# Performance work log

Hardware: AMD Instinct MI355X
Metric: run time of the kernel (lower is better)

The kernel has to match this reference:

```python
import jax, jax.numpy as jnp
import numpy as np
from jax import lax


def setup_inputs() -> dict:
    key = jax.random.key(0)
    k1, k2 = jax.random.split(key)
    B, H, W, Cin, Cout, kh, kw = 16, 128, 128, 128, 128, 3, 3
    X = jax.random.normal(k1, (B, H, W, Cin), dtype=jnp.float32)
    kernel = jax.random.normal(k2, (B, kh, kw, Cin, Cout), dtype=jnp.float32) * 0.05
    return {"X": X, "kernel": kernel}


def _conv_one(x, k):
    # x: [H, W, Cin]; k: [kh, kw, Cin, Cout] -> [H', W', Cout]
    out = lax.conv_general_dilated(
        x[None],  # [1, H, W, Cin]
        k,
        window_strides=(1, 1),
        padding='VALID',
        dimension_numbers=('NHWC', 'HWIO', 'NHWC'),
    )
    return out[0]


def reference(X, kernel):
    # Per-sample dynamic-filter conv: each batch element convolved with its own
    # [kh, kw, Cin, Cout] filter. Equivalent to the TF depthwise-reshape trick
    # followed by reduce_sum over the input-channel axis.
    return jax.vmap(_conv_one)(X, kernel)  # [B, H', W', Cout]
```

## Files before the change

kernel.cpp:

```cpp
#include <hip/hip_runtime.h>
#include <cstdint>

#define OWD 126
#define MTOT 15876

typedef short bf16x8 __attribute__((ext_vector_type(8)));
typedef float f32x4  __attribute__((ext_vector_type(4)));

__device__ __forceinline__ uint16_t f2bf(float f) {
    union { float f; uint32_t u; } v;
    v.f = f;
    uint32_t u = v.u;
    return (uint16_t)((u + 0x7FFFu + ((u >> 16) & 1u)) >> 16);
}

__device__ __forceinline__ uint32_t pk2(float a, float b) {
    return (uint32_t)f2bf(a) | ((uint32_t)f2bf(b) << 16);
}

__global__ __launch_bounds__(256) void kprep(const float* __restrict__ Kin,
                                             uint16_t* __restrict__ Bt) {
    const int rs = blockIdx.x;
    const int b  = blockIdx.y;
    const int t  = threadIdx.x;
    const int n  = t & 127;
    const int og = t >> 7;

    const float* src = Kin + (((size_t)b * 9 + rs) << 14);
    uint16_t*    dst = Bt + ((size_t)b * 128 + n) * 1152 + rs * 128;

#pragma unroll
    for (int o = 0; o < 8; ++o) {
        const int oct = og * 8 + o;
        const float* s0 = src + (oct * 8) * 128 + n;
        uint4 p;
        p.x = pk2(s0[0 * 128], s0[1 * 128]);
        p.y = pk2(s0[2 * 128], s0[3 * 128]);
        p.z = pk2(s0[4 * 128], s0[5 * 128]);
        p.w = pk2(s0[6 * 128], s0[7 * 128]);
        *(uint4*)(dst + oct * 8) = p;
    }
}

__global__ __launch_bounds__(256) void conv_mfma(const float* __restrict__ X,
                                                 const uint16_t* __restrict__ Bt,
                                                 float* __restrict__ Out) {
    __shared__ __align__(16) uint16_t lA[128 * 64];
    __shared__ __align__(16) uint16_t lB[128 * 64];

    const int mtile = blockIdx.x;
    const int b     = blockIdx.y;
    const int tid   = threadIdx.x;
    const int lane  = tid & 63;
    const int wave  = tid >> 6;
    const int wm    = (wave & 1) << 6;
    const int wn    = (wave >> 1) << 6;
    const int l15   = lane & 15;
    const int quad  = lane >> 4;

    const int srow  = tid >> 1;
    const int shalf = tid & 1;

    int m = mtile * 128 + srow;
    if (m >= MTOT) m = MTOT - 1;
    const int oh = m / OWD;
    const int ow = m - oh * OWD;
    const float*    Xb = X + (((size_t)b * 128 + oh) * 128 + ow) * 128;
    const uint16_t* Bb = Bt + ((size_t)b * 128 + srow) * 1152 + shalf * 32;

    f32x4 acc[4][4];
#pragma unroll
    for (int i = 0; i < 4; ++i)
#pragma unroll
        for (int j = 0; j < 4; ++j)
            acc[i][j] = (f32x4){0.f, 0.f, 0.f, 0.f};

    for (int chunk = 0; chunk < 18; ++chunk) {
        const int rs = chunk >> 1;
        const int c0 = (chunk & 1) << 6;
        const int r  = rs / 3;
        const int s  = rs - r * 3;

        __syncthreads();

        {
            const float4* src = (const float4*)(Xb + (r * 128 + s) * 128 + c0 + shalf * 32);
            float4 v[8];
#pragma unroll
            for (int i = 0; i < 8; ++i) v[i] = src[i];
#pragma unroll
            for (int i = 0; i < 4; ++i) {
                uint4 p;
                p.x = pk2(v[2 * i].x, v[2 * i].y);
                p.y = pk2(v[2 * i].z, v[2 * i].w);
                p.z = pk2(v[2 * i + 1].x, v[2 * i + 1].y);
                p.w = pk2(v[2 * i + 1].z, v[2 * i + 1].w);
                const int ci = (shalf * 4 + i) ^ (srow & 7);
                *(uint4*)&lA[srow * 64 + ci * 8] = p;
            }
        }
        {
            const uint4* bsrc = (const uint4*)(Bb + rs * 128 + c0);
#pragma unroll
            for (int i = 0; i < 4; ++i) {
                const uint4 p = bsrc[i];
                const int ci = (shalf * 4 + i) ^ (srow & 7);
                *(uint4*)&lB[srow * 64 + ci * 8] = p;
            }
        }

        __syncthreads();

#pragma unroll
        for (int ksub = 0; ksub < 2; ++ksub) {
            bf16x8 af[4], bfr[4];
#pragma unroll
            for (int i = 0; i < 4; ++i) {
                const int row = wm + i * 16 + l15;
                const int ci  = (ksub * 4 + quad) ^ (row & 7);
                af[i] = *(const bf16x8*)&lA[row * 64 + ci * 8];
            }
#pragma unroll
            for (int j = 0; j < 4; ++j) {
                const int row = wn + j * 16 + l15;
                const int ci  = (ksub * 4 + quad) ^ (row & 7);
                bfr[j] = *(const bf16x8*)&lB[row * 64 + ci * 8];
            }
#pragma unroll
            for (int i = 0; i < 4; ++i)
#pragma unroll
                for (int j = 0; j < 4; ++j)
                    acc[i][j] = __builtin_amdgcn_mfma_f32_16x16x32_bf16(
                        af[i], bfr[j], acc[i][j], 0, 0, 0);
        }
    }

#pragma unroll
    for (int i = 0; i < 4; ++i) {
#pragma unroll
        for (int rr = 0; rr < 4; ++rr) {
            const int mrow = mtile * 128 + wm + i * 16 + quad * 4 + rr;
            if (mrow < MTOT) {
                const int oh2 = mrow / OWD;
                const int ow2 = mrow - oh2 * OWD;
                float* op = Out + (((size_t)b * OWD + oh2) * OWD + ow2) * 128 + wn + l15;
#pragma unroll
                for (int j = 0; j < 4; ++j)
                    op[j * 16] = acc[i][j][rr];
            }
        }
    }
}

extern "C" void kernel_launch(void* const* d_in, const int* in_sizes, int n_in,
                              void* d_out, int out_size, void* d_ws, size_t ws_size,
                              hipStream_t stream) {
    const float* X   = (const float*)d_in[0];
    const float* Kin = (const float*)d_in[1];
    float*       Out = (float*)d_out;
    uint16_t*    Bt  = (uint16_t*)d_ws;

    kprep<<<dim3(9, 16), 256, 0, stream>>>(Kin, Bt);
    conv_mfma<<<dim3(125, 16), 256, 0, stream>>>(X, Bt, Out);
}
```

Measured before the change: 387.0 us.

## Pre-convert X to bf16 and stream tiles via global_load_lds

```diff
diff --git a/kernel.cpp b/kernel.cpp
--- a/kernel.cpp
+++ b/kernel.cpp
@@ -6,6 +6,10 @@
 
 typedef short bf16x8 __attribute__((ext_vector_type(8)));
 typedef float f32x4  __attribute__((ext_vector_type(4)));
+
+#define BT_ELEMS  (16u * 128u * 1152u)
+#define XBF_ELEMS (16u * 128u * 128u * 128u)
+#define WS_NEEDED ((size_t)(BT_ELEMS + XBF_ELEMS) * 2)
 
 __device__ __forceinline__ uint16_t f2bf(float f) {
     union { float f; uint32_t u; } v;
@@ -16,6 +20,12 @@
 
 __device__ __forceinline__ uint32_t pk2(float a, float b) {
     return (uint32_t)f2bf(a) | ((uint32_t)f2bf(b) << 16);
+}
+
+__device__ __forceinline__ void gl_lds16(const uint16_t* g, uint16_t* l) {
+    __builtin_amdgcn_global_load_lds(
+        (const __attribute__((address_space(1))) uint32_t*)g,
+        (__attribute__((address_space(3))) uint32_t*)l, 16, 0, 0);
 }
 
 __global__ __launch_bounds__(256) void kprep(const float* __restrict__ Kin,
@@ -42,11 +52,24 @@
     }
 }
 
-__global__ __launch_bounds__(256) void conv_mfma(const float* __restrict__ X,
-                                                 const uint16_t* __restrict__ Bt,
-                                                 float* __restrict__ Out) {
-    __shared__ __align__(16) uint16_t lA[128 * 64];
-    __shared__ __align__(16) uint16_t lB[128 * 64];
+__global__ __launch_bounds__(256) void xprep(const float* __restrict__ X,
+                                             uint16_t* __restrict__ Xbf) {
+    const size_t i = ((size_t)blockIdx.x * 256 + threadIdx.x) * 8;
+    const float4 a = *(const float4*)(X + i);
+    const float4 b = *(const float4*)(X + i + 4);
+    uint4 p;
+    p.x = pk2(a.x, a.y);
+    p.y = pk2(a.z, a.w);
+    p.z = pk2(b.x, b.y);
+    p.w = pk2(b.z, b.w);
+    *(uint4*)(Xbf + i) = p;
+}
+
+__global__ __launch_bounds__(256) void conv_mfma_a(const uint16_t* __restrict__ Xbf,
+                                                   const uint16_t* __restrict__ Bt,
+                                                   float* __restrict__ Out) {
+    __shared__ __align__(16) uint16_t lA[128 * 32];
+    __shared__ __align__(16) uint16_t lB[128 * 32];
 
     const int mtile = blockIdx.x;
     const int b     = blockIdx.y;
@@ -58,6 +81,96 @@
     const int l15   = lane & 15;
     const int quad  = lane >> 4;
 
+    const int row = tid >> 2;
+    const int kq  = tid & 3;
+
+    int m0 = mtile * 128 + row;        if (m0 >= MTOT) m0 = MTOT - 1;
+    int m1 = mtile * 128 + 64 + row;   if (m1 >= MTOT) m1 = MTOT - 1;
+    const int oh0 = m0 / OWD, ow0 = m0 - oh0 * OWD;
+    const int oh1 = m1 / OWD, ow1 = m1 - oh1 * OWD;
+
+    const uint16_t* Xr0 = Xbf + (((size_t)b * 128 + oh0) * 128 + ow0) * 128 + kq * 8;
+    const uint16_t* Xr1 = Xbf + (((size_t)b * 128 + oh1) * 128 + ow1) * 128 + kq * 8;
+    const uint16_t* Br0 = Bt + ((size_t)b * 128 + row) * 1152 + kq * 8;
+    const uint16_t* Br1 = Bt + ((size_t)b * 128 + 64 + row) * 1152 + kq * 8;
+
+    uint16_t* lA0 = &lA[tid * 8];
+    uint16_t* lA1 = &lA[2048 + tid * 8];
+    uint16_t* lB0 = &lB[tid * 8];
+    uint16_t* lB1 = &lB[2048 + tid * 8];
+
+    f32x4 acc[4][4];
+#pragma unroll
+    for (int i = 0; i < 4; ++i)
+#pragma unroll
+        for (int j = 0; j < 4; ++j)
+            acc[i][j] = (f32x4){0.f, 0.f, 0.f, 0.f};
+
+    for (int rs = 0; rs < 9; ++rs) {
+        const int r = rs / 3;
+        const int s = rs - r * 3;
+        const int aoff0 = (r * 128 + s) * 128;
+        const int boff0 = rs * 128;
+#pragma unroll
+        for (int cs = 0; cs < 4; ++cs) {
+            const int c0 = cs * 32;
+
+            __syncthreads();
+            gl_lds16(Xr0 + aoff0 + c0, lA0);
+            gl_lds16(Xr1 + aoff0 + c0, lA1);
+            gl_lds16(Br0 + boff0 + c0, lB0);
+            gl_lds16(Br1 + boff0 + c0, lB1);
+            __syncthreads();
+
+            bf16x8 af[4], bfr[4];
+#pragma unroll
+            for (int i = 0; i < 4; ++i)
+                af[i] = *(const bf16x8*)&lA[(wm + i * 16 + l15) * 32 + quad * 8];
+#pragma unroll
+            for (int j = 0; j < 4; ++j)
+                bfr[j] = *(const bf16x8*)&lB[(wn + j * 16 + l15) * 32 + quad * 8];
+#pragma unroll
+            for (int i = 0; i < 4; ++i)
+#pragma unroll
+                for (int j = 0; j < 4; ++j)
+                    acc[i][j] = __builtin_amdgcn_mfma_f32_16x16x32_bf16(
+                        af[i], bfr[j], acc[i][j], 0, 0, 0);
+        }
+    }
+
+#pragma unroll
+    for (int i = 0; i < 4; ++i) {
+#pragma unroll
+        for (int rr = 0; rr < 4; ++rr) {
+            const int mrow = mtile * 128 + wm + i * 16 + quad * 4 + rr;
+            if (mrow < MTOT) {
+                const int oh2 = mrow / OWD;
+                const int ow2 = mrow - oh2 * OWD;
+                float* op = Out + (((size_t)b * OWD + oh2) * OWD + ow2) * 128 + wn + l15;
+#pragma unroll
+                for (int j = 0; j < 4; ++j)
+                    op[j * 16] = acc[i][j][rr];
+            }
+        }
+    }
+}
+
+__global__ __launch_bounds__(256) void conv_mfma(const float* __restrict__ X,
+                                                 const uint16_t* __restrict__ Bt,
+                                                 float* __restrict__ Out) {
+    __shared__ __align__(16) uint16_t lA[128 * 64];
+    __shared__ __align__(16) uint16_t lB[128 * 64];
+
+    const int mtile = blockIdx.x;
+    const int b     = blockIdx.y;
+    const int tid   = threadIdx.x;
+    const int lane  = tid & 63;
+    const int wave  = tid >> 6;
+    const int wm    = (wave & 1) << 6;
+    const int wn    = (wave >> 1) << 6;
+    const int l15   = lane & 15;
+    const int quad  = lane >> 4;
+
     const int srow  = tid >> 1;
     const int shalf = tid & 1;
 
@@ -82,7 +195,6 @@
         const int s  = rs - r * 3;
 
         __syncthreads();
-
         {
             const float4* src = (const float4*)(Xb + (r * 128 + s) * 128 + c0 + shalf * 32);
             float4 v[8];
@@ -108,7 +220,6 @@
                 *(uint4*)&lB[srow * 64 + ci * 8] = p;
             }
         }
-
         __syncthreads();
 
 #pragma unroll
@@ -159,7 +270,13 @@
     const float* Kin = (const float*)d_in[1];
     float*       Out = (float*)d_out;
     uint16_t*    Bt  = (uint16_t*)d_ws;
+    uint16_t*    Xbf = Bt + BT_ELEMS;
 
     kprep<<<dim3(9, 16), 256, 0, stream>>>(Kin, Bt);
-    conv_mfma<<<dim3(125, 16), 256, 0, stream>>>(X, Bt, Out);
-}
+    if (ws_size >= WS_NEEDED) {
+        xprep<<<XBF_ELEMS / (256 * 8), 256, 0, stream>>>(X, Xbf);
+        conv_mfma_a<<<dim3(125, 16), 256, 0, stream>>>(Xbf, Bt, Out);
+    } else {
+        conv_mfma<<<dim3(125, 16), 256, 0, stream>>>(X, Bt, Out);
+    }
+}
```

After: 345.0 us. 1.12x faster.
